# Kernel optimization log

Hardware: AMD Instinct MI355X
Metric: run time of the kernel (lower is better)

The kernel has to match this reference:

```python
import jax, jax.numpy as jnp
import numpy as np

EPS = 1e-5  # LayerNorm eps (torch default)
K_NN = 16   # matches init kwarg k


def _knn_idx(pos, k):
    # pos: (B,N,3) -> (B,N,k) indices of k nearest points (sorted by distance,
    # includes self at slot 0), matching pytorch3d knn_points(return_sorted=True).
    sq = jnp.sum(pos * pos, axis=-1)                                   # (B,N)
    d2 = sq[:, :, None] + sq[:, None, :] - 2.0 * jnp.einsum('bnd,bmd->bnm', pos, pos)
    _, idx = jax.lax.top_k(-d2, k)                                     # ascending distance
    return idx


def _gather(feats, idx):
    # feats: (B,N,C), idx: (B,N,K) -> (B,N,K,C)
    return jax.vmap(lambda f, i: f[i])(feats, idx)


def _ln(x, g, b):
    mu = jnp.mean(x, axis=-1, keepdims=True)
    var = jnp.mean((x - mu) ** 2, axis=-1, keepdims=True)
    return (x - mu) * jax.lax.rsqrt(var + EPS) * g + b


def setup_inputs() -> dict:
    key = jax.random.key(0)
    B, N, D, H = 2, 4096, 128, 12
    ks = jax.random.split(key, 16)
    s = 0.05
    f32 = jnp.float32
    return {
        'x': jax.random.normal(ks[0], (B, N, D), f32),
        'pos': jax.random.normal(ks[1], (B, N, 3), f32),
        # linear projections (bias=False)
        'w_q': jax.random.normal(ks[2], (D, D), f32) * s,
        'w_k': jax.random.normal(ks[3], (D, D), f32) * s,
        'w_v': jax.random.normal(ks[4], (D, D), f32) * s,
        # pos_mlp: Linear(3,H) -> LN(H) -> ReLU -> Linear(H,D)
        'pos_w1': jax.random.normal(ks[5], (H, 3), f32) * s,
        'pos_b1': jnp.zeros((H,), f32),
        'pos_g': jnp.ones((H,), f32),
        'pos_beta': jnp.zeros((H,), f32),
        'pos_w2': jax.random.normal(ks[6], (D, H), f32) * s,
        'pos_b2': jnp.zeros((D,), f32),
        # attn_mlp: Linear(D,D) -> LN(D) -> ReLU -> Linear(D,D)
        'attn_w1': jax.random.normal(ks[7], (D, D), f32) * s,
        'attn_b1': jnp.zeros((D,), f32),
        'attn_g': jnp.ones((D,), f32),
        'attn_beta': jnp.zeros((D,), f32),
        'attn_w2': jax.random.normal(ks[8], (D, D), f32) * s,
        'attn_b2': jnp.zeros((D,), f32),
    }


def reference(x, pos, w_q, w_k, w_v,
              pos_w1, pos_b1, pos_g, pos_beta, pos_w2, pos_b2,
              attn_w1, attn_b1, attn_g, attn_beta, attn_w2, attn_b2):
    idx = _knn_idx(pos, K_NN)                        # (B,N,K)
    q = x @ w_q.T                                    # (B,N,D)
    kf = _gather(x @ w_k.T, idx)                     # (B,N,K,D)
    vf = _gather(x @ w_v.T, idx)                     # (B,N,K,D)
    pos_rel = pos[:, :, None, :] - _gather(pos, idx)  # (B,N,K,3)
    # pos_mlp
    pe = _ln(pos_rel @ pos_w1.T + pos_b1, pos_g, pos_beta)
    pe = jax.nn.relu(pe) @ pos_w2.T + pos_b2         # (B,N,K,D)
    # attn_mlp on (q - k + pos_enc)
    w = q[:, :, None, :] - kf + pe
    w = _ln(w @ attn_w1.T + attn_b1, attn_g, attn_beta)
    w = jax.nn.relu(w) @ attn_w2.T + attn_b2         # (B,N,K,D)
    attn = jax.nn.softmax(w, axis=2)                 # softmax over neighbor dim
    return jnp.einsum('bnkd,bnkd->bnd', attn, vf + pe)
```

## Files before the change

kernel.cpp:

```cpp
#include <hip/hip_runtime.h>
#include <hip/hip_bf16.h>
#include <math.h>

#define BATCH 2
#define NPTS 4096
#define DIM 128
#define HID 12
#define KNN 16
#define NSLOT 24
#define BCAP 192
#define BCT 64

#define FOLD_BLOCKS 128
#define M1_BLOCKS 32
#define PRE_BLOCKS (FOLD_BLOCKS + M1_BLOCKS + 4)
#define KNN_BLOCKS (BATCH * NPTS / 4)

typedef __attribute__((ext_vector_type(8))) short short8;
typedef __attribute__((ext_vector_type(4))) float f32x4;

__device__ __forceinline__ short f2b(float f) {
  unsigned u = __float_as_uint(f);
  unsigned r = (u + 0x7fffu + ((u >> 16) & 1u)) >> 16;
  return (short)r;
}
__device__ __forceinline__ float b2f(short h) {
  return __uint_as_float(((unsigned)(unsigned short)h) << 16);
}

#define BITONIC64(v, vi)                                                     \
  {                                                                          \
    _Pragma("unroll") for (int k_ = 2; k_ <= 64; k_ <<= 1) {                 \
      _Pragma("unroll") for (int j_ = k_ >> 1; j_ >= 1; j_ >>= 1) {          \
        const float ov_ = __shfl_xor((v), j_);                               \
        const int oi_ = __shfl_xor((vi), j_);                                \
        const bool up_ = ((lane & k_) == 0);                                 \
        const bool lowpos_ = ((lane & j_) == 0);                             \
        const bool keep_min_ = (lowpos_ == up_);                             \
        const bool lt_ = (ov_ < (v)) || (ov_ == (v) && oi_ < (vi));          \
        const bool take_ = keep_min_ ? lt_ : !lt_;                           \
        if (take_) { (v) = ov_; (vi) = oi_; }                                \
      }                                                                      \
    }                                                                        \
  }

__device__ void knn_body(int bid, const float* __restrict__ pos,
                         int* __restrict__ knn_out) {
  __shared__ float bd_s[4][BCAP];
  __shared__ int bi_s[4][BCAP];

  const int t = threadIdx.x;
  const int w = t >> 6;
  const int lane = t & 63;
  const int n = (bid << 2) + w;
  const int b = n >> 12;
  const int qn = n & (NPTS - 1);

  float* bdl = &bd_s[w][0];
  int* bil = &bi_s[w][0];

  const float* pb = pos + b * NPTS * 3;
  const float qx = pb[qn * 3 + 0];
  const float qy = pb[qn * 3 + 1];
  const float qz = pb[qn * 3 + 2];

  const bool is_slot = (lane < NSLOT);
  float vald, thr;
  int validx;
  int bcount = 0;

  {
    const float2* pp = (const float2*)(pb + lane * 6);
    const float2 u0 = pp[0], u1 = pp[1], u2 = pp[2];
    float dx = qx - u0.x, dy = qy - u0.y, dz = qz - u1.x;
    float v = fmaf(dx, dx, fmaf(dy, dy, dz * dz));
    int vi = lane * 2;
    dx = qx - u1.y; dy = qy - u2.x; dz = qz - u2.y;
    const float d2b = fmaf(dx, dx, fmaf(dy, dy, dz * dz));

    BITONIC64(v, vi)
    vald = is_slot ? v : __builtin_inff();
    validx = is_slot ? vi : 0x7fffffff;
    const float v15 = __shfl(v, 15);
    thr = v15 + v15 * 1e-5f;

    const unsigned long long m = __ballot(d2b < thr);
    if (m) {
      const unsigned lt = __builtin_amdgcn_mbcnt_hi(
          (unsigned)(m >> 32), __builtin_amdgcn_mbcnt_lo((unsigned)m, 0u));
      if (d2b < thr) { bdl[lt] = d2b; bil[lt] = 2 * lane + 1; }
      bcount = (int)__builtin_popcountll(m);
    }
  }

  const float2* pp = (const float2*)(pb + 384 + lane * 6);
  float2 A0 = pp[0], A1 = pp[1], A2 = pp[2];
  pp = (const float2*)(pb + 768 + lane * 6);
  float2 B0 = pp[0], B1 = pp[1], B2 = pp[2];

#pragma unroll 1
  for (int it = 1; it < NPTS / 128; ++it) {
    const float2 c0 = A0, c1v = A1, c2 = A2;
    A0 = B0; A1 = B1; A2 = B2;
    if (it + 2 < NPTS / 128) {
      pp = (const float2*)(pb + (it + 2) * 384 + lane * 6);
      B0 = pp[0]; B1 = pp[1]; B2 = pp[2];
    }
    float dx = qx - c0.x, dy = qy - c0.y, dz = qz - c1v.x;
    const float e2a = fmaf(dx, dx, fmaf(dy, dy, dz * dz));
    dx = qx - c1v.y; dy = qy - c2.x; dz = qz - c2.y;
    const float e2b = fmaf(dx, dx, fmaf(dy, dy, dz * dz));

    if (bcount >= BCT) {
#pragma unroll 1
      while (bcount > 0) {
        const int take = bcount < 40 ? bcount : 40;
        float mv = __builtin_inff();
        int mi = 0x7fffffff;
        if (lane < NSLOT) { mv = vald; mi = validx; }
        else if (lane - NSLOT < take) {
          mv = bdl[bcount - take + lane - NSLOT];
          mi = bil[bcount - take + lane - NSLOT];
        }
        BITONIC64(mv, mi)
        if (is_slot) { vald = mv; validx = mi; }
        bcount -= take;
      }
      const float v15 = __shfl(vald, 15);
      thr = v15 + v15 * 1e-5f;
    }

    {
      const unsigned long long m = __ballot(e2a < thr);
      if (m) {
        const unsigned lt = __builtin_amdgcn_mbcnt_hi(
            (unsigned)(m >> 32), __builtin_amdgcn_mbcnt_lo((unsigned)m, 0u));
        if (e2a < thr) { bdl[bcount + lt] = e2a; bil[bcount + lt] = it * 128 + 2 * lane; }
        bcount += (int)__builtin_popcountll(m);
      }
    }
    {
      const unsigned long long m = __ballot(e2b < thr);
      if (m) {
        const unsigned lt = __builtin_amdgcn_mbcnt_hi(
            (unsigned)(m >> 32), __builtin_amdgcn_mbcnt_lo((unsigned)m, 0u));
        if (e2b < thr) { bdl[bcount + lt] = e2b; bil[bcount + lt] = it * 128 + 2 * lane + 1; }
        bcount += (int)__builtin_popcountll(m);
      }
    }
  }

#pragma unroll 1
  while (bcount > 0) {
    const int take = bcount < 40 ? bcount : 40;
    float mv = __builtin_inff();
    int mi = 0x7fffffff;
    if (lane < NSLOT) { mv = vald; mi = validx; }
    else if (lane - NSLOT < take) {
      mv = bdl[bcount - take + lane - NSLOT];
      mi = bil[bcount - take + lane - NSLOT];
    }
    BITONIC64(mv, mi)
    if (is_slot) { vald = mv; validx = mi; }
    bcount -= take;
  }

  double d2e = 1e300;
  if (is_slot) {
    const double ex = (double)qx - (double)pb[validx * 3 + 0];
    const double ey = (double)qy - (double)pb[validx * 3 + 1];
    const double ez = (double)qz - (double)pb[validx * 3 + 2];
    d2e = ex * ex + ey * ey + ez * ez;
  }
  int rank = 0;
#pragma unroll 1
  for (int j = 0; j < NSLOT; ++j) {
    const double dj = __shfl(d2e, j);
    const int ij = __shfl(validx, j);
    if (dj < d2e || (dj == d2e && ij < validx)) ++rank;
  }
  if (is_slot && rank < KNN) knn_out[((b << 12) + qn) * KNN + rank] = validx;
}

__device__ void fold_body(int bid, const float* __restrict__ aw1,
                          const float* __restrict__ wq, const float* __restrict__ wk,
                          short* __restrict__ WqaHi, short* __restrict__ WqaLo,
                          short* __restrict__ WkaHi, short* __restrict__ WkaLo) {
  const float* w = (bid < 64) ? wq : wk;
  short* oh = (bid < 64) ? WqaHi : WkaHi;
  short* ol = (bid < 64) ? WqaLo : WkaLo;
  const int row = ((bid & 63) << 1) + (threadIdx.x >> 7);
  const int i = threadIdx.x & 127;
  float acc = 0.f;
  for (int j = 0; j < 128; ++j) acc = fmaf(aw1[row * 128 + j], w[j * 128 + i], acc);
  const short h = f2b(acc);
  oh[row * 128 + i] = h;
  ol[row * 128 + i] = f2b(acc - b2f(h));
}

__device__ void m1_body(int bid, const float* __restrict__ aw1,
                        const float* __restrict__ pw2, const float* __restrict__ pb2,
                        const float* __restrict__ ab1,
                        short* __restrict__ M1b, float* __restrict__ c1) {
  const int t = threadIdx.x;
  const int wid = t >> 6, lane = t & 63;
  const int o = bid * 4 + wid;
  const float a0 = aw1[o * 128 + lane];
  const float a1 = aw1[o * 128 + 64 + lane];

  float s = fmaf(a0, pb2[lane], a1 * pb2[64 + lane]);
#pragma unroll
  for (int off = 1; off < 64; off <<= 1) s += __shfl_xor(s, off);
  if (lane == 0) c1[o] = ab1[o] + s;

#pragma unroll
  for (int k = 0; k < HID; ++k) {
    float p = fmaf(a0, pw2[lane * HID + k], a1 * pw2[(64 + lane) * HID + k]);
#pragma unroll
    for (int off = 1; off < 64; off <<= 1) p += __shfl_xor(p, off);
    if (lane == 0) M1b[o * 32 + k] = f2b(p);
  }
  if (lane >= HID && lane < 32) M1b[o * 32 + lane] = 0;
}

__device__ void pw2b_body(const float* __restrict__ pw2, short* __restrict__ pw2b) {
  const int t = threadIdx.x;
  for (int i = t; i < 128 * 32; i += 256) {
    const int o = i >> 5, k = i & 31;
    pw2b[i] = (k < HID) ? f2b(pw2[o * HID + k]) : (short)0;
  }
}
__device__ void aw2b_body(int half, const float* __restrict__ aw2,
                          short* __restrict__ aw2b) {
  const int base = half * 8192;
  for (int i = threadIdx.x; i < 8192; i += 256) aw2b[base + i] = f2b(aw2[base + i]);
}
__device__ void wv_body(const float* __restrict__ wv, short* __restrict__ WvHi,
                        short* __restrict__ WvLo) {
  for (int i = threadIdx.x; i < 128 * 128; i += 256) {
    const float v = wv[i];
    const short h = f2b(v);
    WvHi[i] = h;
    WvLo[i] = f2b(v - b2f(h));
  }
}

__global__ __launch_bounds__(256) void knn_prep_kernel(
    const float* __restrict__ pos, int* __restrict__ knn_out,
    const float* __restrict__ aw1, const float* __restrict__ wq,
    const float* __restrict__ wk,
    short* __restrict__ WqaHi, short* __restrict__ WqaLo,
    short* __restrict__ WkaHi, short* __restrict__ WkaLo,
    const float* __restrict__ pw2, const float* __restrict__ pb2,
    const float* __restrict__ ab1, const float* __restrict__ aw2,
    const float* __restrict__ wv,
    short* __restrict__ M1b, short* __restrict__ pw2b, short* __restrict__ aw2b,
    float* __restrict__ c1, short* __restrict__ WvHi, short* __restrict__ WvLo) {
  const int bid = blockIdx.x;
  if (bid < FOLD_BLOCKS) {
    fold_body(bid, aw1, wq, wk, WqaHi, WqaLo, WkaHi, WkaLo);
  } else if (bid < FOLD_BLOCKS + M1_BLOCKS) {
    m1_body(bid - FOLD_BLOCKS, aw1, pw2, pb2, ab1, M1b, c1);
  } else if (bid == FOLD_BLOCKS + M1_BLOCKS) {
    pw2b_body(pw2, pw2b);
  } else if (bid <= FOLD_BLOCKS + M1_BLOCKS + 2) {
    aw2b_body(bid - (FOLD_BLOCKS + M1_BLOCKS + 1), aw2, aw2b);
  } else if (bid == FOLD_BLOCKS + M1_BLOCKS + 3) {
    wv_body(wv, WvHi, WvLo);
  } else {
    knn_body(bid - PRE_BLOCKS, pos, knn_out);
  }
}

__global__ __launch_bounds__(256) void proj_mfma_kernel(
    const float* __restrict__ x,
    const short* __restrict__ WqaHi, const short* __restrict__ WqaLo,
    const short* __restrict__ WkaHi, const short* __restrict__ WkaLo,
    const short* __restrict__ WvHi, const short* __restrict__ WvLo,
    short* __restrict__ QAb, short* __restrict__ KAb, short* __restrict__ Vpb) {
  const int t = threadIdx.x;
  const int wid = t >> 6, lane = t & 63;
  const int r16 = lane & 15, g4 = lane >> 4;
  const int rowbase = blockIdx.x * 32 + (wid >> 1) * 16;
  const int ch = wid & 1;

  short8 ahi[4], alo[4];
#pragma unroll
  for (int ks = 0; ks < 4; ++ks) {
    const float* xp = x + (rowbase + r16) * DIM + ks * 32 + g4 * 8;
#pragma unroll
    for (int e = 0; e < 8; ++e) {
      const float v = xp[e];
      const short h = f2b(v);
      ahi[ks][e] = h;
      alo[ks][e] = f2b(v - b2f(h));
    }
  }

  const f32x4 zero4 = {0.f, 0.f, 0.f, 0.f};
  const short* WH[3] = {WqaHi, WkaHi, WvHi};
  const short* WL[3] = {WqaLo, WkaLo, WvLo};
  short* OUT[3] = {QAb, KAb, Vpb};
#pragma unroll
  for (int mi = 0; mi < 3; ++mi) {
    const short* wh = WH[mi];
    const short* wl = WL[mi];
    short* o = OUT[mi];
#pragma unroll
    for (int q = 0; q < 4; ++q) {
      const int col = (ch * 4 + q) * 16 + r16;
      f32x4 a = zero4;
#pragma unroll
      for (int ks = 0; ks < 4; ++ks) {
        const short8 bh = *(const short8*)(wh + col * DIM + ks * 32 + g4 * 8);
        const short8 bl = *(const short8*)(wl + col * DIM + ks * 32 + g4 * 8);
        a = __builtin_amdgcn_mfma_f32_16x16x32_bf16(ahi[ks], bh, a, 0, 0, 0);
        a = __builtin_amdgcn_mfma_f32_16x16x32_bf16(alo[ks], bh, a, 0, 0, 0);
        a = __builtin_amdgcn_mfma_f32_16x16x32_bf16(ahi[ks], bl, a, 0, 0, 0);
      }
#pragma unroll
      for (int reg = 0; reg < 4; ++reg)
        o[(rowbase + g4 * 4 + reg) * DIM + (ch * 4 + q) * 16 + r16] = f2b(a[reg]);
    }
  }
}

__global__ __launch_bounds__(256) void pt_wave_kernel(
    const float* __restrict__ pos, const int* __restrict__ knn_in,
    const short* __restrict__ QAb, const short* __restrict__ KAb,
    const short* __restrict__ Vpb,
    const float* __restrict__ pw1, const float* __restrict__ pb1,
    const float* __restrict__ pg, const float* __restrict__ pbeta,
    const float* __restrict__ pb2,
    const float* __restrict__ ag, const float* __restrict__ abeta,
    const float* __restrict__ ab2, const float* __restrict__ c1,
    const short* __restrict__ M1b, const short* __restrict__ pw2b,
    const short* __restrict__ aw2b,
    float* __restrict__ out) {
  __shared__ __align__(16) short z_s[2048];
  __shared__ float red_s[2][4][16];

  const int t = threadIdx.x;
  const int wid = t >> 6;
  const int lane = t & 63;
  const int r16 = lane & 15;
  const int g4 = lane >> 4;
  const int n = blockIdx.x;
  const int b = n >> 12;

  int myidx = 0;
  if (lane < KNN) myidx = knn_in[n * KNN + lane];
  const int jA = __shfl(myidx, r16);
  int jC[4];
#pragma unroll
  for (int reg = 0; reg < 4; ++reg) jC[reg] = __shfl(myidx, g4 * 4 + reg);

  const int ja_g = b * NPTS + jA;
  const float pjx = pos[ja_g * 3 + 0];
  const float pjy = pos[ja_g * 3 + 1];
  const float pjz = pos[ja_g * 3 + 2];
  const float qx = pos[n * 3 + 0], qy = pos[n * 3 + 1], qz = pos[n * 3 + 2];

  float qa_[2], kav[2][4], vv[2][4];
#pragma unroll
  for (int q = 0; q < 2; ++q) {
    const int o = (wid * 2 + q) * 16 + r16;
    qa_[q] = b2f(QAb[n * DIM + o]);
#pragma unroll
    for (int reg = 0; reg < 4; ++reg) {
      const int row = b * NPTS + jC[reg];
      kav[q][reg] = b2f(KAb[row * DIM + o]);
      vv[q][reg] = b2f(Vpb[row * DIM + o]);
    }
  }

  const float rx = qx - pjx, ry = qy - pjy, rz = qz - pjz;
  float hr[HID];
  {
    float mu = 0.f;
#pragma unroll
    for (int hh = 0; hh < HID; ++hh) {
      const float v = pb1[hh] + rx * pw1[hh * 3 + 0] + ry * pw1[hh * 3 + 1] +
                      rz * pw1[hh * 3 + 2];
      hr[hh] = v;
      mu += v;
    }
    mu *= (1.f / HID);
    float var = 0.f;
#pragma unroll
    for (int hh = 0; hh < HID; ++hh) { const float d = hr[hh] - mu; var = fmaf(d, d, var); }
    const float rs = rsqrtf(var * (1.f / HID) + 1e-5f);
#pragma unroll
    for (int hh = 0; hh < HID; ++hh)
      hr[hh] = fmaxf(fmaf((hr[hh] - mu) * rs, pg[hh], pbeta[hh]), 0.f);
  }

  short8 a1 = {0, 0, 0, 0, 0, 0, 0, 0};
  if (g4 == 0) {
#pragma unroll
    for (int e = 0; e < 8; ++e) a1[e] = f2b(hr[e]);
  } else if (g4 == 1) {
#pragma unroll
    for (int e = 0; e < 4; ++e) a1[e] = f2b(hr[8 + e]);
  }

  const f32x4 zero4 = {0.f, 0.f, 0.f, 0.f};
  f32x4 accw[2], accp[2];
#pragma unroll
  for (int q = 0; q < 2; ++q) {
    const int boff = ((wid * 2 + q) * 16 + r16) * 32 + g4 * 8;
    const short8 bm = *(const short8*)(M1b + boff);
    const short8 bp = *(const short8*)(pw2b + boff);
    accw[q] = __builtin_amdgcn_mfma_f32_16x16x32_bf16(a1, bm, zero4, 0, 0, 0);
    accp[q] = __builtin_amdgcn_mfma_f32_16x16x32_bf16(a1, bp, zero4, 0, 0, 0);
  }

  float w1v[2][4];
#pragma unroll
  for (int q = 0; q < 2; ++q) {
    const int o = (wid * 2 + q) * 16 + r16;
    const float base = qa_[q] + c1[o];
#pragma unroll
    for (int reg = 0; reg < 4; ++reg)
      w1v[q][reg] = accw[q][reg] + base - kav[q][reg];
  }

  {
    float ps[4], pq2[4];
#pragma unroll
    for (int reg = 0; reg < 4; ++reg) {
      ps[reg] = w1v[0][reg] + w1v[1][reg];
      pq2[reg] = fmaf(w1v[0][reg], w1v[0][reg], w1v[1][reg] * w1v[1][reg]);
    }
#pragma unroll
    for (int reg = 0; reg < 4; ++reg) {
#pragma unroll
      for (int off = 1; off <= 8; off <<= 1) {
        ps[reg] += __shfl_xor(ps[reg], off);
        pq2[reg] += __shfl_xor(pq2[reg], off);
      }
    }
    if (r16 == 0) {
#pragma unroll
      for (int reg = 0; reg < 4; ++reg) {
        red_s[0][wid][g4 * 4 + reg] = ps[reg];
        red_s[1][wid][g4 * 4 + reg] = pq2[reg];
      }
    }
  }
  __syncthreads();
  float mu[4], rs[4];
#pragma unroll
  for (int reg = 0; reg < 4; ++reg) {
    const int rr = g4 * 4 + reg;
    const float s = red_s[0][0][rr] + red_s[0][1][rr] + red_s[0][2][rr] + red_s[0][3][rr];
    const float q2 = red_s[1][0][rr] + red_s[1][1][rr] + red_s[1][2][rr] + red_s[1][3][rr];
    mu[reg] = s * (1.f / 128.f);
    const float var = q2 * (1.f / 128.f) - mu[reg] * mu[reg];
    rs[reg] = rsqrtf(var + 1e-5f);
  }

  {
    char* zb = (char*)z_s;
#pragma unroll
    for (int q = 0; q < 2; ++q) {
      const int o = (wid * 2 + q) * 16 + r16;
      const float gam = ag[o], bet = abeta[o];
#pragma unroll
      for (int reg = 0; reg < 4; ++reg) {
        const int rr = g4 * 4 + reg;
        const float zv = fmaxf(fmaf((w1v[q][reg] - mu[reg]) * rs[reg], gam, bet), 0.f);
        unsigned byte = (unsigned)(rr * 256 + o * 2);
        byte ^= ((unsigned)(rr & 7) << 4) ^ ((unsigned)(rr & 8) << 2);
        *(short*)(zb + byte) = f2b(zv);
      }
    }
  }
  __syncthreads();

  short8 a2[4];
  {
    const char* zb = (const char*)z_s;
#pragma unroll
    for (int ks = 0; ks < 4; ++ks) {
      unsigned byte = (unsigned)(r16 * 256 + ks * 64 + g4 * 16);
      byte ^= ((unsigned)(r16 & 7) << 4) ^ ((unsigned)(r16 & 8) << 2);
      a2[ks] = *(const short8*)(zb + byte);
    }
  }

  f32x4 acc2[2] = {zero4, zero4};
#pragma unroll
  for (int q = 0; q < 2; ++q) {
#pragma unroll
    for (int ks = 0; ks < 4; ++ks) {
      const short8 bw =
          *(const short8*)(aw2b + ((wid * 2 + q) * 16 + r16) * DIM + ks * 32 + g4 * 8);
      acc2[q] = __builtin_amdgcn_mfma_f32_16x16x32_bf16(a2[ks], bw, acc2[q], 0, 0, 0);
    }
  }

  float ew[2][4], inv[2];
#pragma unroll
  for (int q = 0; q < 2; ++q) {
    const float bb = ab2[(wid * 2 + q) * 16 + r16];
#pragma unroll
    for (int reg = 0; reg < 4; ++reg) ew[q][reg] = acc2[q][reg] + bb;
    float m = fmaxf(fmaxf(ew[q][0], ew[q][1]), fmaxf(ew[q][2], ew[q][3]));
    m = fmaxf(m, __shfl_xor(m, 16));
    m = fmaxf(m, __shfl_xor(m, 32));
    float s = 0.f;
#pragma unroll
    for (int reg = 0; reg < 4; ++reg) { ew[q][reg] = __expf(ew[q][reg] - m); s += ew[q][reg]; }
    s += __shfl_xor(s, 16);
    s += __shfl_xor(s, 32);
    inv[q] = 1.f / s;
  }

  float o_acc[2];
#pragma unroll
  for (int q = 0; q < 2; ++q) {
    const int o = (wid * 2 + q) * 16 + r16;
    const float pb = pb2[o];
    float acc = 0.f;
#pragma unroll
    for (int reg = 0; reg < 4; ++reg)
      acc = fmaf(ew[q][reg] * inv[q], vv[q][reg] + accp[q][reg] + pb, acc);
    acc += __shfl_xor(acc, 16);
    acc += __shfl_xor(acc, 32);
    o_acc[q] = acc;
  }
  if (g4 < 2) out[n * DIM + (wid * 2 + g4) * 16 + r16] = o_acc[g4];
}

extern "C" void kernel_launch(void* const* d_in, const int* in_sizes, int n_in,
                              void* d_out, int out_size, void* d_ws, size_t ws_size,
                              hipStream_t stream) {
  const float* x   = (const float*)d_in[0];
  const float* pos = (const float*)d_in[1];
  const float* wq  = (const float*)d_in[2];
  const float* wk  = (const float*)d_in[3];
  const float* wv  = (const float*)d_in[4];
  const float* pw1 = (const float*)d_in[5];
  const float* pb1 = (const float*)d_in[6];
  const float* pg  = (const float*)d_in[7];
  const float* pbt = (const float*)d_in[8];
  const float* pw2 = (const float*)d_in[9];
  const float* pb2 = (const float*)d_in[10];
  const float* aw1 = (const float*)d_in[11];
  const float* ab1 = (const float*)d_in[12];
  const float* ag  = (const float*)d_in[13];
  const float* abt = (const float*)d_in[14];
  const float* aw2 = (const float*)d_in[15];
  const float* ab2 = (const float*)d_in[16];
  float* out = (float*)d_out;

  char* ws = (char*)d_ws;
  int*   knn   = (int*)ws;
  short* WqaHi = (short*)(ws + 512u * 1024u);
  short* WqaLo = (short*)(ws + 544u * 1024u);
  short* WkaHi = (short*)(ws + 576u * 1024u);
  short* WkaLo = (short*)(ws + 608u * 1024u);
  short* M1b   = (short*)(ws + 640u * 1024u);
  short* pw2b  = (short*)(ws + 648u * 1024u);
  short* aw2b  = (short*)(ws + 656u * 1024u);
  float* c1    = (float*)(ws + 688u * 1024u);
  short* WvHi  = (short*)(ws + 704u * 1024u);
  short* WvLo  = (short*)(ws + 736u * 1024u);
  short* QAb   = (short*)(ws + (1u << 20));
  short* KAb   = (short*)(ws + 4u * (1u << 20));
  short* Vpb   = (short*)(ws + 7u * (1u << 20));

  knn_prep_kernel<<<PRE_BLOCKS + KNN_BLOCKS, 256, 0, stream>>>(
      pos, knn, aw1, wq, wk, WqaHi, WqaLo, WkaHi, WkaLo, pw2, pb2, ab1, aw2, wv,
      M1b, pw2b, aw2b, c1, WvHi, WvLo);
  proj_mfma_kernel<<<BATCH * NPTS / 32, 256, 0, stream>>>(
      x, WqaHi, WqaLo, WkaHi, WkaLo, WvHi, WvLo, QAb, KAb, Vpb);
  pt_wave_kernel<<<BATCH * NPTS, 256, 0, stream>>>(
      pos, knn, QAb, KAb, Vpb, pw1, pb1, pg, pbt, pb2, ag, abt, ab2, c1, M1b, pw2b, aw2b, out);
}
```

Measured before the change: 120.4 us.

## Move kNN into projection kernel and software-pipeline gathers across four points per block

```diff
diff --git a/kernel.cpp b/kernel.cpp
--- a/kernel.cpp
+++ b/kernel.cpp
@@ -13,7 +13,8 @@
 
 #define FOLD_BLOCKS 128
 #define M1_BLOCKS 32
-#define PRE_BLOCKS (FOLD_BLOCKS + M1_BLOCKS + 4)
+#define PREP_BLOCKS (FOLD_BLOCKS + M1_BLOCKS + 4)
+#define PROJ_BLOCKS (BATCH * NPTS / 32)
 #define KNN_BLOCKS (BATCH * NPTS / 4)
 
 typedef __attribute__((ext_vector_type(8))) short short8;
@@ -245,8 +246,7 @@
   }
 }
 
-__global__ __launch_bounds__(256) void knn_prep_kernel(
-    const float* __restrict__ pos, int* __restrict__ knn_out,
+__global__ __launch_bounds__(256) void prep_kernel(
     const float* __restrict__ aw1, const float* __restrict__ wq,
     const float* __restrict__ wk,
     short* __restrict__ WqaHi, short* __restrict__ WqaLo,
@@ -265,23 +265,21 @@
     pw2b_body(pw2, pw2b);
   } else if (bid <= FOLD_BLOCKS + M1_BLOCKS + 2) {
     aw2b_body(bid - (FOLD_BLOCKS + M1_BLOCKS + 1), aw2, aw2b);
-  } else if (bid == FOLD_BLOCKS + M1_BLOCKS + 3) {
+  } else {
     wv_body(wv, WvHi, WvLo);
-  } else {
-    knn_body(bid - PRE_BLOCKS, pos, knn_out);
-  }
-}
-
-__global__ __launch_bounds__(256) void proj_mfma_kernel(
-    const float* __restrict__ x,
-    const short* __restrict__ WqaHi, const short* __restrict__ WqaLo,
-    const short* __restrict__ WkaHi, const short* __restrict__ WkaLo,
-    const short* __restrict__ WvHi, const short* __restrict__ WvLo,
-    short* __restrict__ QAb, short* __restrict__ KAb, short* __restrict__ Vpb) {
+  }
+}
+
+__device__ void proj_body(int bid, const float* __restrict__ x,
+                          const short* __restrict__ WqaHi, const short* __restrict__ WqaLo,
+                          const short* __restrict__ WkaHi, const short* __restrict__ WkaLo,
+                          const short* __restrict__ WvHi, const short* __restrict__ WvLo,
+                          short* __restrict__ QAb, short* __restrict__ KAb,
+                          short* __restrict__ Vpb) {
   const int t = threadIdx.x;
   const int wid = t >> 6, lane = t & 63;
   const int r16 = lane & 15, g4 = lane >> 4;
-  const int rowbase = blockIdx.x * 32 + (wid >> 1) * 16;
+  const int rowbase = bid * 32 + (wid >> 1) * 16;
   const int ch = wid & 1;
 
   short8 ahi[4], alo[4];
@@ -321,6 +319,51 @@
 #pragma unroll
       for (int reg = 0; reg < 4; ++reg)
         o[(rowbase + g4 * 4 + reg) * DIM + (ch * 4 + q) * 16 + r16] = f2b(a[reg]);
+    }
+  }
+}
+
+__global__ __launch_bounds__(256) void knn_proj_kernel(
+    const float* __restrict__ pos, int* __restrict__ knn_out,
+    const float* __restrict__ x,
+    const short* __restrict__ WqaHi, const short* __restrict__ WqaLo,
+    const short* __restrict__ WkaHi, const short* __restrict__ WkaLo,
+    const short* __restrict__ WvHi, const short* __restrict__ WvLo,
+    short* __restrict__ QAb, short* __restrict__ KAb, short* __restrict__ Vpb) {
+  const int bid = blockIdx.x;
+  if (bid < PROJ_BLOCKS) {
+    proj_body(bid, x, WqaHi, WqaLo, WkaHi, WkaLo, WvHi, WvLo, QAb, KAb, Vpb);
+  } else {
+    knn_body(bid - PROJ_BLOCKS, pos, knn_out);
+  }
+}
+
+struct GRegs {
+  float pj[3], q[3];
+  float qa[2];
+  float kav[2][4];
+  float vv[2][4];
+};
+
+__device__ __forceinline__ void issue_gathers(
+    int n, int b, int jA, const int* jC, int wid, int r16,
+    const float* __restrict__ pos, const short* __restrict__ QAb,
+    const short* __restrict__ KAb, const short* __restrict__ Vpb, GRegs& g) {
+  const int ja_g = b * NPTS + jA;
+#pragma unroll
+  for (int c = 0; c < 3; ++c) {
+    g.pj[c] = pos[ja_g * 3 + c];
+    g.q[c] = pos[n * 3 + c];
+  }
+#pragma unroll
+  for (int q = 0; q < 2; ++q) {
+    const int o = (wid * 2 + q) * 16 + r16;
+    g.qa[q] = b2f(QAb[n * DIM + o]);
+#pragma unroll
+    for (int reg = 0; reg < 4; ++reg) {
+      const int row = b * NPTS + jC[reg];
+      g.kav[q][reg] = b2f(KAb[row * DIM + o]);
+      g.vv[q][reg] = b2f(Vpb[row * DIM + o]);
     }
   }
 }
@@ -345,192 +388,198 @@
   const int lane = t & 63;
   const int r16 = lane & 15;
   const int g4 = lane >> 4;
-  const int n = blockIdx.x;
-  const int b = n >> 12;
-
-  int myidx = 0;
-  if (lane < KNN) myidx = knn_in[n * KNN + lane];
-  const int jA = __shfl(myidx, r16);
-  int jC[4];
-#pragma unroll
-  for (int reg = 0; reg < 4; ++reg) jC[reg] = __shfl(myidx, g4 * 4 + reg);
-
-  const int ja_g = b * NPTS + jA;
-  const float pjx = pos[ja_g * 3 + 0];
-  const float pjy = pos[ja_g * 3 + 1];
-  const float pjz = pos[ja_g * 3 + 2];
-  const float qx = pos[n * 3 + 0], qy = pos[n * 3 + 1], qz = pos[n * 3 + 2];
-
-  float qa_[2], kav[2][4], vv[2][4];
-#pragma unroll
-  for (int q = 0; q < 2; ++q) {
-    const int o = (wid * 2 + q) * 16 + r16;
-    qa_[q] = b2f(QAb[n * DIM + o]);
-#pragma unroll
-    for (int reg = 0; reg < 4; ++reg) {
-      const int row = b * NPTS + jC[reg];
-      kav[q][reg] = b2f(KAb[row * DIM + o]);
-      vv[q][reg] = b2f(Vpb[row * DIM + o]);
-    }
-  }
-
-  const float rx = qx - pjx, ry = qy - pjy, rz = qz - pjz;
-  float hr[HID];
+  const int n0 = blockIdx.x * 4;
+  const int b = n0 >> 12;
+
+  GRegs cur, nxt;
   {
-    float mu = 0.f;
-#pragma unroll
-    for (int hh = 0; hh < HID; ++hh) {
-      const float v = pb1[hh] + rx * pw1[hh * 3 + 0] + ry * pw1[hh * 3 + 1] +
-                      rz * pw1[hh * 3 + 2];
-      hr[hh] = v;
-      mu += v;
-    }
-    mu *= (1.f / HID);
-    float var = 0.f;
-#pragma unroll
-    for (int hh = 0; hh < HID; ++hh) { const float d = hr[hh] - mu; var = fmaf(d, d, var); }
-    const float rs = rsqrtf(var * (1.f / HID) + 1e-5f);
-#pragma unroll
-    for (int hh = 0; hh < HID; ++hh)
-      hr[hh] = fmaxf(fmaf((hr[hh] - mu) * rs, pg[hh], pbeta[hh]), 0.f);
-  }
-
-  short8 a1 = {0, 0, 0, 0, 0, 0, 0, 0};
-  if (g4 == 0) {
-#pragma unroll
-    for (int e = 0; e < 8; ++e) a1[e] = f2b(hr[e]);
-  } else if (g4 == 1) {
-#pragma unroll
-    for (int e = 0; e < 4; ++e) a1[e] = f2b(hr[8 + e]);
+    int m0 = 0;
+    if (lane < KNN) m0 = knn_in[n0 * KNN + lane];
+    const int jA = __shfl(m0, r16);
+    int jC[4];
+#pragma unroll
+    for (int reg = 0; reg < 4; ++reg) jC[reg] = __shfl(m0, g4 * 4 + reg);
+    issue_gathers(n0, b, jA, jC, wid, r16, pos, QAb, KAb, Vpb, cur);
   }
 
   const f32x4 zero4 = {0.f, 0.f, 0.f, 0.f};
-  f32x4 accw[2], accp[2];
-#pragma unroll
-  for (int q = 0; q < 2; ++q) {
-    const int boff = ((wid * 2 + q) * 16 + r16) * 32 + g4 * 8;
-    const short8 bm = *(const short8*)(M1b + boff);
-    const short8 bp = *(const short8*)(pw2b + boff);
-    accw[q] = __builtin_amdgcn_mfma_f32_16x16x32_bf16(a1, bm, zero4, 0, 0, 0);
-    accp[q] = __builtin_amdgcn_mfma_f32_16x16x32_bf16(a1, bp, zero4, 0, 0, 0);
-  }
-
-  float w1v[2][4];
-#pragma unroll
-  for (int q = 0; q < 2; ++q) {
-    const int o = (wid * 2 + q) * 16 + r16;
-    const float base = qa_[q] + c1[o];
-#pragma unroll
-    for (int reg = 0; reg < 4; ++reg)
-      w1v[q][reg] = accw[q][reg] + base - kav[q][reg];
-  }
-
-  {
-    float ps[4], pq2[4];
-#pragma unroll
-    for (int reg = 0; reg < 4; ++reg) {
-      ps[reg] = w1v[0][reg] + w1v[1][reg];
-      pq2[reg] = fmaf(w1v[0][reg], w1v[0][reg], w1v[1][reg] * w1v[1][reg]);
-    }
-#pragma unroll
-    for (int reg = 0; reg < 4; ++reg) {
-#pragma unroll
-      for (int off = 1; off <= 8; off <<= 1) {
-        ps[reg] += __shfl_xor(ps[reg], off);
-        pq2[reg] += __shfl_xor(pq2[reg], off);
-      }
-    }
-    if (r16 == 0) {
-#pragma unroll
-      for (int reg = 0; reg < 4; ++reg) {
-        red_s[0][wid][g4 * 4 + reg] = ps[reg];
-        red_s[1][wid][g4 * 4 + reg] = pq2[reg];
-      }
-    }
-  }
-  __syncthreads();
-  float mu[4], rs[4];
-#pragma unroll
-  for (int reg = 0; reg < 4; ++reg) {
-    const int rr = g4 * 4 + reg;
-    const float s = red_s[0][0][rr] + red_s[0][1][rr] + red_s[0][2][rr] + red_s[0][3][rr];
-    const float q2 = red_s[1][0][rr] + red_s[1][1][rr] + red_s[1][2][rr] + red_s[1][3][rr];
-    mu[reg] = s * (1.f / 128.f);
-    const float var = q2 * (1.f / 128.f) - mu[reg] * mu[reg];
-    rs[reg] = rsqrtf(var + 1e-5f);
-  }
-
-  {
-    char* zb = (char*)z_s;
+
+#pragma unroll
+  for (int i = 0; i < 4; ++i) {
+    const int n = n0 + i;
+
+    int mN = 0;
+    if (i < 3 && lane < KNN) mN = knn_in[(n + 1) * KNN + lane];
+
+    const float rx = cur.q[0] - cur.pj[0];
+    const float ry = cur.q[1] - cur.pj[1];
+    const float rz = cur.q[2] - cur.pj[2];
+    float hr[HID];
+    {
+      float mu = 0.f;
+#pragma unroll
+      for (int hh = 0; hh < HID; ++hh) {
+        const float v = pb1[hh] + rx * pw1[hh * 3 + 0] + ry * pw1[hh * 3 + 1] +
+                        rz * pw1[hh * 3 + 2];
+        hr[hh] = v;
+        mu += v;
+      }
+      mu *= (1.f / HID);
+      float var = 0.f;
+#pragma unroll
+      for (int hh = 0; hh < HID; ++hh) { const float d = hr[hh] - mu; var = fmaf(d, d, var); }
+      const float rsn = rsqrtf(var * (1.f / HID) + 1e-5f);
+#pragma unroll
+      for (int hh = 0; hh < HID; ++hh)
+        hr[hh] = fmaxf(fmaf((hr[hh] - mu) * rsn, pg[hh], pbeta[hh]), 0.f);
+    }
+
+    short8 a1 = {0, 0, 0, 0, 0, 0, 0, 0};
+    if (g4 == 0) {
+#pragma unroll
+      for (int e = 0; e < 8; ++e) a1[e] = f2b(hr[e]);
+    } else if (g4 == 1) {
+#pragma unroll
+      for (int e = 0; e < 4; ++e) a1[e] = f2b(hr[8 + e]);
+    }
+
+    if (i < 3) {
+      const int jAN = __shfl(mN, r16);
+      int jCN[4];
+#pragma unroll
+      for (int reg = 0; reg < 4; ++reg) jCN[reg] = __shfl(mN, g4 * 4 + reg);
+      issue_gathers(n + 1, b, jAN, jCN, wid, r16, pos, QAb, KAb, Vpb, nxt);
+    }
+
+    f32x4 accw[2], accp[2];
+#pragma unroll
+    for (int q = 0; q < 2; ++q) {
+      const int boff = ((wid * 2 + q) * 16 + r16) * 32 + g4 * 8;
+      const short8 bm = *(const short8*)(M1b + boff);
+      const short8 bp = *(const short8*)(pw2b + boff);
+      accw[q] = __builtin_amdgcn_mfma_f32_16x16x32_bf16(a1, bm, zero4, 0, 0, 0);
+      accp[q] = __builtin_amdgcn_mfma_f32_16x16x32_bf16(a1, bp, zero4, 0, 0, 0);
+    }
+
+    float w1v[2][4];
 #pragma unroll
     for (int q = 0; q < 2; ++q) {
       const int o = (wid * 2 + q) * 16 + r16;
-      const float gam = ag[o], bet = abeta[o];
+      const float base = cur.qa[q] + c1[o];
+#pragma unroll
+      for (int reg = 0; reg < 4; ++reg)
+        w1v[q][reg] = accw[q][reg] + base - cur.kav[q][reg];
+    }
+
+    {
+      float ps[4], pq2[4];
 #pragma unroll
       for (int reg = 0; reg < 4; ++reg) {
-        const int rr = g4 * 4 + reg;
-        const float zv = fmaxf(fmaf((w1v[q][reg] - mu[reg]) * rs[reg], gam, bet), 0.f);
-        unsigned byte = (unsigned)(rr * 256 + o * 2);
-        byte ^= ((unsigned)(rr & 7) << 4) ^ ((unsigned)(rr & 8) << 2);
-        *(short*)(zb + byte) = f2b(zv);
-      }
-    }
-  }
-  __syncthreads();
-
-  short8 a2[4];
-  {
-    const char* zb = (const char*)z_s;
-#pragma unroll
-    for (int ks = 0; ks < 4; ++ks) {
-      unsigned byte = (unsigned)(r16 * 256 + ks * 64 + g4 * 16);
-      byte ^= ((unsigned)(r16 & 7) << 4) ^ ((unsigned)(r16 & 8) << 2);
-      a2[ks] = *(const short8*)(zb + byte);
-    }
-  }
-
-  f32x4 acc2[2] = {zero4, zero4};
-#pragma unroll
-  for (int q = 0; q < 2; ++q) {
-#pragma unroll
-    for (int ks = 0; ks < 4; ++ks) {
-      const short8 bw =
-          *(const short8*)(aw2b + ((wid * 2 + q) * 16 + r16) * DIM + ks * 32 + g4 * 8);
-      acc2[q] = __builtin_amdgcn_mfma_f32_16x16x32_bf16(a2[ks], bw, acc2[q], 0, 0, 0);
-    }
-  }
-
-  float ew[2][4], inv[2];
-#pragma unroll
-  for (int q = 0; q < 2; ++q) {
-    const float bb = ab2[(wid * 2 + q) * 16 + r16];
-#pragma unroll
-    for (int reg = 0; reg < 4; ++reg) ew[q][reg] = acc2[q][reg] + bb;
-    float m = fmaxf(fmaxf(ew[q][0], ew[q][1]), fmaxf(ew[q][2], ew[q][3]));
-    m = fmaxf(m, __shfl_xor(m, 16));
-    m = fmaxf(m, __shfl_xor(m, 32));
-    float s = 0.f;
-#pragma unroll
-    for (int reg = 0; reg < 4; ++reg) { ew[q][reg] = __expf(ew[q][reg] - m); s += ew[q][reg]; }
-    s += __shfl_xor(s, 16);
-    s += __shfl_xor(s, 32);
-    inv[q] = 1.f / s;
-  }
-
-  float o_acc[2];
-#pragma unroll
-  for (int q = 0; q < 2; ++q) {
-    const int o = (wid * 2 + q) * 16 + r16;
-    const float pb = pb2[o];
-    float acc = 0.f;
-#pragma unroll
-    for (int reg = 0; reg < 4; ++reg)
-      acc = fmaf(ew[q][reg] * inv[q], vv[q][reg] + accp[q][reg] + pb, acc);
-    acc += __shfl_xor(acc, 16);
-    acc += __shfl_xor(acc, 32);
-    o_acc[q] = acc;
-  }
-  if (g4 < 2) out[n * DIM + (wid * 2 + g4) * 16 + r16] = o_acc[g4];
+        ps[reg] = w1v[0][reg] + w1v[1][reg];
+        pq2[reg] = fmaf(w1v[0][reg], w1v[0][reg], w1v[1][reg] * w1v[1][reg]);
+      }
+#pragma unroll
+      for (int reg = 0; reg < 4; ++reg) {
+#pragma unroll
+        for (int off = 1; off <= 8; off <<= 1) {
+          ps[reg] += __shfl_xor(ps[reg], off);
+          pq2[reg] += __shfl_xor(pq2[reg], off);
+        }
+      }
+      if (r16 == 0) {
+#pragma unroll
+        for (int reg = 0; reg < 4; ++reg) {
+          red_s[0][wid][g4 * 4 + reg] = ps[reg];
+          red_s[1][wid][g4 * 4 + reg] = pq2[reg];
+        }
+      }
+    }
+    __syncthreads();
+    float mu[4], rsv[4];
+#pragma unroll
+    for (int reg = 0; reg < 4; ++reg) {
+      const int rr = g4 * 4 + reg;
+      const float s = red_s[0][0][rr] + red_s[0][1][rr] + red_s[0][2][rr] + red_s[0][3][rr];
+      const float q2 = red_s[1][0][rr] + red_s[1][1][rr] + red_s[1][2][rr] + red_s[1][3][rr];
+      mu[reg] = s * (1.f / 128.f);
+      const float var = q2 * (1.f / 128.f) - mu[reg] * mu[reg];
+      rsv[reg] = rsqrtf(var + 1e-5f);
+    }
+
+    {
+      char* zb = (char*)z_s;
+#pragma unroll
+      for (int q = 0; q < 2; ++q) {
+        const int o = (wid * 2 + q) * 16 + r16;
+        const float gam = ag[o], bet = abeta[o];
+#pragma unroll
+        for (int reg = 0; reg < 4; ++reg) {
+          const int rr = g4 * 4 + reg;
+          const float zv = fmaxf(fmaf((w1v[q][reg] - mu[reg]) * rsv[reg], gam, bet), 0.f);
+          unsigned byte = (unsigned)(rr * 256 + o * 2);
+          byte ^= ((unsigned)(rr & 7) << 4) ^ ((unsigned)(rr & 8) << 2);
+          *(short*)(zb + byte) = f2b(zv);
+        }
+      }
+    }
+    __syncthreads();
+
+    short8 a2[4];
+    {
+      const char* zb = (const char*)z_s;
+#pragma unroll
+      for (int ks = 0; ks < 4; ++ks) {
+        unsigned byte = (unsigned)(r16 * 256 + ks * 64 + g4 * 16);
+        byte ^= ((unsigned)(r16 & 7) << 4) ^ ((unsigned)(r16 & 8) << 2);
+        a2[ks] = *(const short8*)(zb + byte);
+      }
+    }
+
+    f32x4 acc2[2] = {zero4, zero4};
+#pragma unroll
+    for (int q = 0; q < 2; ++q) {
+#pragma unroll
+      for (int ks = 0; ks < 4; ++ks) {
+        const short8 bw =
+            *(const short8*)(aw2b + ((wid * 2 + q) * 16 + r16) * DIM + ks * 32 + g4 * 8);
+        acc2[q] = __builtin_amdgcn_mfma_f32_16x16x32_bf16(a2[ks], bw, acc2[q], 0, 0, 0);
+      }
+    }
+
+    float ew[2][4], inv[2];
+#pragma unroll
+    for (int q = 0; q < 2; ++q) {
+      const float bb = ab2[(wid * 2 + q) * 16 + r16];
+#pragma unroll
+      for (int reg = 0; reg < 4; ++reg) ew[q][reg] = acc2[q][reg] + bb;
+      float m = fmaxf(fmaxf(ew[q][0], ew[q][1]), fmaxf(ew[q][2], ew[q][3]));
+      m = fmaxf(m, __shfl_xor(m, 16));
+      m = fmaxf(m, __shfl_xor(m, 32));
+      float s = 0.f;
+#pragma unroll
+      for (int reg = 0; reg < 4; ++reg) { ew[q][reg] = __expf(ew[q][reg] - m); s += ew[q][reg]; }
+      s += __shfl_xor(s, 16);
+      s += __shfl_xor(s, 32);
+      inv[q] = 1.f / s;
+    }
+
+    float o_acc[2];
+#pragma unroll
+    for (int q = 0; q < 2; ++q) {
+      const int o = (wid * 2 + q) * 16 + r16;
+      const float pb = pb2[o];
+      float acc = 0.f;
+#pragma unroll
+      for (int reg = 0; reg < 4; ++reg)
+        acc = fmaf(ew[q][reg] * inv[q], cur.vv[q][reg] + accp[q][reg] + pb, acc);
+      acc += __shfl_xor(acc, 16);
+      acc += __shfl_xor(acc, 32);
+      o_acc[q] = acc;
+    }
+    if (g4 < 2) out[n * DIM + (wid * 2 + g4) * 16 + r16] = o_acc[g4];
+
+    if (i < 3) cur = nxt;
+  }
 }
 
 extern "C" void kernel_launch(void* const* d_in, const int* in_sizes, int n_in,
@@ -571,11 +620,12 @@
   short* KAb   = (short*)(ws + 4u * (1u << 20));
   short* Vpb   = (short*)(ws + 7u * (1u << 20));
 
-  knn_prep_kernel<<<PRE_BLOCKS + KNN_BLOCKS, 256, 0, stream>>>(
-      pos, knn, aw1, wq, wk, WqaHi, WqaLo, WkaHi, WkaLo, pw2, pb2, ab1, aw2, wv,
+  prep_kernel<<<PREP_BLOCKS, 256, 0, stream>>>(
+      aw1, wq, wk, WqaHi, WqaLo, WkaHi, WkaLo, pw2, pb2, ab1, aw2, wv,
       M1b, pw2b, aw2b, c1, WvHi, WvLo);
-  proj_mfma_kernel<<<BATCH * NPTS / 32, 256, 0, stream>>>(
-      x, WqaHi, WqaLo, WkaHi, WkaLo, WvHi, WvLo, QAb, KAb, Vpb);
-  pt_wave_kernel<<<BATCH * NPTS, 256, 0, stream>>>(
-      pos, knn, QAb, KAb, Vpb, pw1, pb1, pg, pbt, pb2, ag, abt, ab2, c1, M1b, pw2b, aw2b, out);
-}
+  knn_proj_kernel<<<PROJ_BLOCKS + KNN_BLOCKS, 256, 0, stream>>>(
+      pos, knn, x, WqaHi, WqaLo, WkaHi, WkaLo, WvHi, WvLo, QAb, KAb, Vpb);
+  pt_wave_kernel<<<BATCH * NPTS / 4, 256, 0, stream>>>(
+      pos, knn, QAb, KAb, Vpb, pw1, pb1, pg, pbt, pb2, ag, abt, ab2, c1,
+      M1b, pw2b, aw2b, out);
+}
```

Measured after the change: 136.2 us. 13.1% more time.
